# Kernel tuning notes

Measured on AMD Instinct MI355X. Metric: run time of the kernel, lower is better.

The kernel has to match this reference:

```python
import jax, jax.numpy as jnp
import numpy as np

B, S, D_MODEL, H = 2, 2048, 1024, 16
DH = D_MODEL // H  # head size = 64
NEG = -1e12


def setup_inputs() -> dict:
    key = jax.random.key(0)
    ks = jax.random.split(key, 10)
    x = jax.random.normal(ks[0], (B, S, D_MODEL), dtype=jnp.float32)
    # realistic padding mask: random valid lengths in [S//2, S]
    lengths = jax.random.randint(ks[1], (B,), S // 2, S + 1)
    mask = jnp.arange(S)[None, :] < lengths[:, None]  # [B, S] bool
    init = 0.02
    Wq = jax.random.normal(ks[2], (D_MODEL, D_MODEL), jnp.float32) * init
    Wk = jax.random.normal(ks[3], (D_MODEL, D_MODEL), jnp.float32) * init
    Wv = jax.random.normal(ks[4], (D_MODEL, D_MODEL), jnp.float32) * init
    Wr = jax.random.normal(ks[5], (D_MODEL, D_MODEL), jnp.float32) * init
    bq = jnp.zeros((D_MODEL,), jnp.float32)
    bk = jnp.zeros((D_MODEL,), jnp.float32)
    bv = jnp.zeros((D_MODEL,), jnp.float32)
    br = jnp.zeros((D_MODEL,), jnp.float32)
    return {"x": x, "mask": mask, "Wq": Wq, "bq": bq, "Wk": Wk, "bk": bk,
            "Wv": Wv, "bv": bv, "Wr": Wr, "br": br}


def reference(x, mask, Wq, bq, Wk, bk, Wv, bv, Wr, br):
    # x: [B,S,D]; mask: [B,S] bool (True = valid token)
    def heads(w, b):
        y = x @ w + b                         # [B,S,D]
        return y.reshape(B, S, H, DH).transpose(0, 2, 1, 3)  # [B,H,S,DH]

    qw, kw, vw = heads(Wq, bq), heads(Wk, bk), heads(Wv, bv)
    scores = jnp.einsum('bhqd,bhkd->bhqk', qw, kw) / jnp.sqrt(jnp.float32(DH))
    # padding mask on key axis ('-inf' fill)
    scores = jnp.where(mask[:, None, None, :], scores, NEG)
    # lm (causal, lower-triangular) additive mask
    causal = jnp.tril(jnp.ones((S, S), dtype=bool))
    scores = scores + jnp.where(causal, 0.0, NEG)[None, None]
    a = jax.nn.softmax(scores, axis=-1)
    o = jnp.einsum('bhqk,bhkd->bhqd', a, vw)          # [B,H,S,DH]
    o = o.transpose(0, 2, 1, 3).reshape(B, S, D_MODEL)  # [B,S,D]
    # second padding mask on output (value=0, sequence axis)
    o = o * mask[:, :, None].astype(o.dtype)
    # residual projection
    o = o + (x @ Wr + br)
    return o
```

## Files before the change

kernel.cpp:

```cpp
#include <hip/hip_runtime.h>
#include <hip/hip_bf16.h>

#define BQ 2
#define SEQ 2048
#define DM 1024
#define NH 16
#define DHEAD 64

typedef unsigned short u16;
typedef unsigned int u32;
typedef __attribute__((ext_vector_type(8))) short short8;
typedef __attribute__((ext_vector_type(4))) float f32x4;

__device__ __forceinline__ u16 f2b(float f) {
    unsigned u = __builtin_bit_cast(unsigned, f);
    unsigned r = u + 0x7fffu + ((u >> 16) & 1u);
    return (u16)(r >> 16);
}

__device__ __forceinline__ void gld_lds16(const void* g, void* l) {
    __builtin_amdgcn_global_load_lds(
        (const __attribute__((address_space(1))) void*)g,
        (__attribute__((address_space(3))) void*)l, 16, 0, 0);
}


__global__ __launch_bounds__(256) void cvt_x_kernel(const float* __restrict__ x,
                                                    u16* __restrict__ xb) {
    int i = blockIdx.x * 256 + threadIdx.x;
    float4 v = ((const float4*)x)[i];
    ushort4 o;
    o.x = f2b(v.x); o.y = f2b(v.y); o.z = f2b(v.z); o.w = f2b(v.w);
    ((ushort4*)xb)[i] = o;
}

__global__ __launch_bounds__(256) void pack_w4(
        const float* __restrict__ W0, const float* __restrict__ W1,
        const float* __restrict__ W2, const float* __restrict__ W3,
        u16* __restrict__ wt) {
    __shared__ u16 Ws[64][68];
    const float* W = (blockIdx.z == 0) ? W0 : (blockIdx.z == 1) ? W1
                   : (blockIdx.z == 2) ? W2 : W3;
    const int k0 = blockIdx.x * 64, d0 = blockIdx.y * 64;
    const int t = threadIdx.x;
    const int lrow = t >> 4, lcol = (t & 15) * 4;
    #pragma unroll
    for (int i = 0; i < 4; i++) {
        float4 v = *(const float4*)(W + (size_t)(k0 + lrow + i * 16) * DM + d0 + lcol);
        Ws[lrow + i * 16][lcol + 0] = f2b(v.x);
        Ws[lrow + i * 16][lcol + 1] = f2b(v.y);
        Ws[lrow + i * 16][lcol + 2] = f2b(v.z);
        Ws[lrow + i * 16][lcol + 3] = f2b(v.w);
    }
    __syncthreads();
    const int dl = t >> 2, kq = (t & 3) * 16;
    uint4 o1, o2;
    o1.x = (u32)Ws[kq + 0][dl]  | ((u32)Ws[kq + 1][dl]  << 16);
    o1.y = (u32)Ws[kq + 2][dl]  | ((u32)Ws[kq + 3][dl]  << 16);
    o1.z = (u32)Ws[kq + 4][dl]  | ((u32)Ws[kq + 5][dl]  << 16);
    o1.w = (u32)Ws[kq + 6][dl]  | ((u32)Ws[kq + 7][dl]  << 16);
    o2.x = (u32)Ws[kq + 8][dl]  | ((u32)Ws[kq + 9][dl]  << 16);
    o2.y = (u32)Ws[kq + 10][dl] | ((u32)Ws[kq + 11][dl] << 16);
    o2.z = (u32)Ws[kq + 12][dl] | ((u32)Ws[kq + 13][dl] << 16);
    o2.w = (u32)Ws[kq + 14][dl] | ((u32)Ws[kq + 15][dl] << 16);
    u16* dst = wt + (size_t)(blockIdx.z * DM + d0 + dl) * DM + k0 + kq;
    *(uint4*)(dst) = o1;
    *(uint4*)(dst + 8) = o2;
}

__global__ __launch_bounds__(256) void pack_bias_kernel(const float* __restrict__ b0,
                                                        const float* __restrict__ b1,
                                                        const float* __restrict__ b2,
                                                        const float* __restrict__ b3,
                                                        float* __restrict__ bias) {
    int i = blockIdx.x * 256 + threadIdx.x;
    const float* s = (i < 1024) ? b0 : (i < 2048) ? b1 : (i < 3072) ? b2 : b3;
    bias[i] = s[i & 1023];
}

__global__ __launch_bounds__(256) void calc_len_kernel(const int* __restrict__ mask,
                                                       int* __restrict__ lengths) {
    __shared__ int cnt[BQ];
    if (threadIdx.x < BQ) cnt[threadIdx.x] = 0;
    __syncthreads();
    for (int b = 0; b < BQ; b++) {
        int c = 0;
        for (int s = threadIdx.x; s < SEQ; s += 256)
            c += (mask[b * SEQ + s] != 0) ? 1 : 0;
        atomicAdd(&cnt[b], c);
    }
    __syncthreads();
    if (threadIdx.x < BQ) lengths[threadIdx.x] = cnt[threadIdx.x];
}


__global__ __launch_bounds__(256) void gemm_qkvr(
        const u16* __restrict__ xb, const u16* __restrict__ wt,
        const float* __restrict__ bias,
        u16* __restrict__ qbuf, u16* __restrict__ kbuf, u16* __restrict__ vbuf,
        float* __restrict__ out) {
    __shared__ __align__(16) u16 As[128 * 32];
    __shared__ __align__(16) u16 Bs[128 * 32];
    const int tid = threadIdx.x;
    const int wid = tid >> 6, lane = tid & 63;
    const int lr = lane & 15, lg = lane >> 4;
    const int bm = blockIdx.x, bn = blockIdx.y;
    const int wm = (wid >> 1) * 64, wn = (wid & 1) * 64;

    const int crow = lane >> 2, ccol = (lane & 3) * 8;
    const u16* agp0 = xb + (size_t)(bm * 128 + (wid * 2 + 0) * 16 + crow) * DM + ccol;
    const u16* agp1 = xb + (size_t)(bm * 128 + (wid * 2 + 1) * 16 + crow) * DM + ccol;
    const u16* bgp0 = wt + (size_t)(bn * 128 + (wid * 2 + 0) * 16 + crow) * DM + ccol;
    const u16* bgp1 = wt + (size_t)(bn * 128 + (wid * 2 + 1) * 16 + crow) * DM + ccol;
    u16* al0 = As + (wid * 2 + 0) * 512;
    u16* al1 = As + (wid * 2 + 1) * 512;
    u16* bl0 = Bs + (wid * 2 + 0) * 512;
    u16* bl1 = Bs + (wid * 2 + 1) * 512;

    f32x4 acc[4][4] = {};

    for (int kk = 0; kk < DM; kk += 32) {
        gld_lds16(agp0 + kk, al0);
        gld_lds16(agp1 + kk, al1);
        gld_lds16(bgp0 + kk, bl0);
        gld_lds16(bgp1 + kk, bl1);
        __syncthreads();
        short8 af[4], bfr[4];
        #pragma unroll
        for (int mt = 0; mt < 4; mt++)
            af[mt] = *(const short8*)(As + (wm + mt * 16 + lr) * 32 + lg * 8);
        #pragma unroll
        for (int nt = 0; nt < 4; nt++)
            bfr[nt] = *(const short8*)(Bs + (wn + nt * 16 + lr) * 32 + lg * 8);
        #pragma unroll
        for (int mt = 0; mt < 4; mt++)
            #pragma unroll
            for (int nt = 0; nt < 4; nt++)
                acc[mt][nt] = __builtin_amdgcn_mfma_f32_16x16x32_bf16(
                        af[mt], bfr[nt], acc[mt][nt], 0, 0, 0);
        __syncthreads();
    }

    #pragma unroll
    for (int nt = 0; nt < 4; nt++) {
        int n = bn * 128 + wn + nt * 16 + lr;
        int which = n >> 10, d = n & 1023;
        float bv_ = bias[n];
        #pragma unroll
        for (int mt = 0; mt < 4; mt++) {
            #pragma unroll
            for (int r = 0; r < 4; r++) {
                int m = bm * 128 + wm + mt * 16 + lg * 4 + r;
                float y = acc[mt][nt][r] + bv_;
                if (which == 3) {
                    out[(size_t)m * DM + d] = y;
                } else {
                    int h = d >> 6, dh = d & 63;
                    int b = m >> 11, s = m & (SEQ - 1);
                    size_t idx = ((size_t)(b * NH + h) * SEQ + s) * DHEAD + dh;
                    u16 hv = f2b(y);
                    if (which == 0) qbuf[idx] = hv;
                    else if (which == 1) kbuf[idx] = hv;
                    else vbuf[idx] = hv;
                }
            }
        }
    }
}


__global__ __launch_bounds__(128) void attn_kernel(
        const u16* __restrict__ qbuf, const u16* __restrict__ kbuf,
        const u16* __restrict__ vbuf, const int* __restrict__ lengths,
        float* __restrict__ out) {
    __shared__ __align__(16) u32 lds[2][64 * 32 + 32 * 32];

    const int wid = threadIdx.x >> 6;
    const int bh = blockIdx.x;
    const int slice = blockIdx.y;
    const int zz = blockIdx.z;
    const int qt = wid ? zz : 15 - zz;
    const int b = bh >> 4, h = bh & 15;
    const int len = lengths[b];
    const int qw = qt * 128 + slice * 32;
    if (qw >= len) return;

    u32* Vt = &lds[wid][0];
    u32* Pl = &lds[wid][2048];

    const int lane = threadIdx.x & 63;
    const int lr = lane & 15, lg = lane >> 4;
    const int swz = (lr & 7) << 2;

    const u16* qp = qbuf + (size_t)bh * SEQ * DHEAD;
    const u16* kp = kbuf + (size_t)bh * SEQ * DHEAD;
    const u16* vp = vbuf + (size_t)bh * SEQ * DHEAD;

    short8 bq[2][2];
    #pragma unroll
    for (int ntq = 0; ntq < 2; ntq++)
        #pragma unroll
        for (int ks = 0; ks < 2; ks++)
            bq[ntq][ks] = *(const short8*)(qp + (size_t)(qw + ntq * 16 + lr) * DHEAD + ks * 32 + lg * 8);

    f32x4 oacc[4][2] = {};
    float mrow[2] = {-3.0e38f, -3.0e38f};
    float lsum[2] = {0.0f, 0.0f};

    const int nkt = (qw >> 6) + 1;
    const int vk = (lane & 31) * 2;
    const int vd0 = (lane >> 5) * 8;
    const float SC = 0.125f * 1.44269504f;

    uint4 vreg[8];
    #pragma unroll
    for (int c = 0; c < 4; c++) {
        const u16* vrow = vp + (size_t)vk * DHEAD + vd0 + c * 16;
        vreg[2 * c]     = *(const uint4*)vrow;
        vreg[2 * c + 1] = *(const uint4*)(vrow + DHEAD);
    }

    for (int kt = 0; kt < nkt; kt++) {
        const int kbase = kt * 64;

        #pragma unroll
        for (int c = 0; c < 4; c++) {
            union { uint4 v; u16 sv[8]; } ua, ub;
            ua.v = vreg[2 * c]; ub.v = vreg[2 * c + 1];
            int d = vd0 + c * 16;
            #pragma unroll
            for (int j = 0; j < 8; j++) {
                u32 w = (u32)ua.sv[j] | ((u32)ub.sv[j] << 16);
                Vt[(d + j) * 32 + ((vk >> 1) ^ (j << 2))] = w;
            }
        }
        if (kt + 1 < nkt) {
            #pragma unroll
            for (int c = 0; c < 4; c++) {
                const u16* vrow = vp + (size_t)(kbase + 64 + vk) * DHEAD + vd0 + c * 16;
                vreg[2 * c]     = *(const uint4*)vrow;
                vreg[2 * c + 1] = *(const uint4*)(vrow + DHEAD);
            }
        }

        short8 ak[4][2];
        #pragma unroll
        for (int mtk = 0; mtk < 4; mtk++)
            #pragma unroll
            for (int ks = 0; ks < 2; ks++)
                ak[mtk][ks] = *(const short8*)(kp + (size_t)(kbase + mtk * 16 + lr) * DHEAD + ks * 32 + lg * 8);
        f32x4 sc[4][2] = {};
        #pragma unroll
        for (int mtk = 0; mtk < 4; mtk++)
            #pragma unroll
            for (int ks = 0; ks < 2; ks++)
                #pragma unroll
                for (int ntq = 0; ntq < 2; ntq++)
                    sc[mtk][ntq] = __builtin_amdgcn_mfma_f32_16x16x32_bf16(
                            ak[mtk][ks], bq[ntq][ks], sc[mtk][ntq], 0, 0, 0);

        const bool maskful = (kbase + 63 > qw);
        if (maskful) {
            #pragma unroll
            for (int mtk = 0; mtk < 4; mtk++) {
                int keyb = kbase + mtk * 16 + lg * 4;
                #pragma unroll
                for (int ntq = 0; ntq < 2; ntq++) {
                    int qq = qw + ntq * 16 + lr;
                    #pragma unroll
                    for (int r = 0; r < 4; r++)
                        sc[mtk][ntq][r] = (keyb + r > qq) ? -3.0e38f
                                                          : sc[mtk][ntq][r] * SC;
                }
            }
        } else {
            #pragma unroll
            for (int mtk = 0; mtk < 4; mtk++)
                #pragma unroll
                for (int ntq = 0; ntq < 2; ntq++)
                    #pragma unroll
                    for (int r = 0; r < 4; r++)
                        sc[mtk][ntq][r] *= SC;
        }

        float scl[2];
        #pragma unroll
        for (int ntq = 0; ntq < 2; ntq++) {
            float mx = sc[0][ntq][0];
            #pragma unroll
            for (int mtk = 0; mtk < 4; mtk++)
                #pragma unroll
                for (int r = 0; r < 4; r++)
                    mx = fmaxf(mx, sc[mtk][ntq][r]);
            mx = fmaxf(mx, __shfl_xor(mx, 16, 64));
            mx = fmaxf(mx, __shfl_xor(mx, 32, 64));
            float mnew = fmaxf(mrow[ntq], mx);
            float sq = exp2f(mrow[ntq] - mnew);
            mrow[ntq] = mnew;
            float ps = 0.0f;
            #pragma unroll
            for (int mtk = 0; mtk < 4; mtk++)
                #pragma unroll
                for (int r = 0; r < 4; r++) {
                    float p = exp2f(sc[mtk][ntq][r] - mnew);
                    sc[mtk][ntq][r] = p;
                    ps += p;
                }
            ps += __shfl_xor(ps, 16, 64);
            ps += __shfl_xor(ps, 32, 64);
            lsum[ntq] = lsum[ntq] * sq + ps;
            scl[ntq] = sq;
        }
        #pragma unroll
        for (int mtd = 0; mtd < 4; mtd++)
            #pragma unroll
            for (int ntq = 0; ntq < 2; ntq++)
                #pragma unroll
                for (int r = 0; r < 4; r++)
                    oacc[mtd][ntq][r] *= scl[ntq];

        #pragma unroll
        for (int ntq = 0; ntq < 2; ntq++) {
            int rowbase = (ntq * 16 + lr) * 32;
            #pragma unroll
            for (int mtk = 0; mtk < 4; mtk++)
                #pragma unroll
                for (int i = 0; i < 2; i++) {
                    u32 w = (u32)f2b(sc[mtk][ntq][2 * i])
                          | ((u32)f2b(sc[mtk][ntq][2 * i + 1]) << 16);
                    Pl[rowbase + ((mtk * 8 + lg * 2 + i) ^ swz)] = w;
                }
        }

        #pragma unroll
        for (int ks = 0; ks < 2; ks++) {
            int wv = (ks * 16 + lg * 4) ^ swz;
            short8 bp0 = *(const short8*)&Pl[(lr) * 32 + wv];
            short8 bp1 = *(const short8*)&Pl[(16 + lr) * 32 + wv];
            #pragma unroll
            for (int mtd = 0; mtd < 4; mtd++) {
                short8 av = *(const short8*)&Vt[(mtd * 16 + lr) * 32 + wv];
                oacc[mtd][0] = __builtin_amdgcn_mfma_f32_16x16x32_bf16(av, bp0, oacc[mtd][0], 0, 0, 0);
                oacc[mtd][1] = __builtin_amdgcn_mfma_f32_16x16x32_bf16(av, bp1, oacc[mtd][1], 0, 0, 0);
            }
        }
    }

    #pragma unroll
    for (int ntq = 0; ntq < 2; ntq++) {
        int q = qw + ntq * 16 + lr;
        if (q < len) {
            float inv = 1.0f / lsum[ntq];
            float* orow = out + (size_t)(b * SEQ + q) * DM + h * DHEAD;
            #pragma unroll
            for (int mtd = 0; mtd < 4; mtd++)
                #pragma unroll
                for (int r = 0; r < 4; r++)
                    orow[mtd * 16 + lg * 4 + r] += oacc[mtd][ntq][r] * inv;
        }
    }
}


extern "C" void kernel_launch(void* const* d_in, const int* in_sizes, int n_in,
                              void* d_out, int out_size, void* d_ws, size_t ws_size,
                              hipStream_t stream) {
    const float* x  = (const float*)d_in[0];
    const int*  mask = (const int*)d_in[1];
    const float* Wq = (const float*)d_in[2];
    const float* bq = (const float*)d_in[3];
    const float* Wk = (const float*)d_in[4];
    const float* bk = (const float*)d_in[5];
    const float* Wv = (const float*)d_in[6];
    const float* bv = (const float*)d_in[7];
    const float* Wr = (const float*)d_in[8];
    const float* br = (const float*)d_in[9];
    float* out = (float*)d_out;

    char* ws = (char*)d_ws;
    size_t off = 0;
    auto alloc = [&](size_t bytes) {
        size_t o = off; off = (off + bytes + 255) & ~(size_t)255; return o;
    };
    u16* xb   = (u16*)(ws + alloc((size_t)BQ * SEQ * DM * 2));
    u16* wt   = (u16*)(ws + alloc((size_t)4 * DM * DM * 2));
    float* bias = (float*)(ws + alloc(4 * DM * 4));
    u16* qbuf = (u16*)(ws + alloc((size_t)BQ * NH * SEQ * DHEAD * 2));
    u16* kbuf = (u16*)(ws + alloc((size_t)BQ * NH * SEQ * DHEAD * 2));
    u16* vbuf = (u16*)(ws + alloc((size_t)BQ * NH * SEQ * DHEAD * 2));
    int* lens = (int*)(ws + alloc(256));

    hipLaunchKernelGGL(cvt_x_kernel, dim3((BQ * SEQ * DM) / 4 / 256), dim3(256), 0, stream, x, xb);
    hipLaunchKernelGGL(pack_w4, dim3(16, 16, 4), dim3(256), 0, stream, Wq, Wk, Wv, Wr, wt);
    hipLaunchKernelGGL(pack_bias_kernel, dim3(16), dim3(256), 0, stream, bq, bk, bv, br, bias);
    hipLaunchKernelGGL(calc_len_kernel, dim3(1), dim3(256), 0, stream, mask, lens);
    hipLaunchKernelGGL(gemm_qkvr, dim3(32, 32), dim3(256), 0, stream,
                       xb, wt, bias, qbuf, kbuf, vbuf, out);
    hipLaunchKernelGGL(attn_kernel, dim3(BQ * NH, 4, 8), dim3(128), 0, stream,
                       qbuf, kbuf, vbuf, lens, out);
}
```

Before: 195.1 us.

## Split attention KV range across four waves with LDS softmax merge

Changes attention from one wave per 32-query tile (paired causal tiles per block) to four waves per 32-query tile, each processing every fourth 64-key block (split-K). The partial outputs, row maxima and row sums are merged through shared memory after a block barrier before the output is written. The grid is also remapped so consecutive block IDs spread (b,h) across XCDs. This shortens the critical path for long causal rows, at the cost of extra LDS traffic, a barrier, and idle waves on short rows.

```diff
diff --git a/kernel.cpp b/kernel.cpp
--- a/kernel.cpp
+++ b/kernel.cpp
@@ -169,28 +169,28 @@
 }
 
 
-__global__ __launch_bounds__(128) void attn_kernel(
+__global__ __launch_bounds__(256) void attn_kernel(
         const u16* __restrict__ qbuf, const u16* __restrict__ kbuf,
         const u16* __restrict__ vbuf, const int* __restrict__ lengths,
         float* __restrict__ out) {
-    __shared__ __align__(16) u32 lds[2][64 * 32 + 32 * 32];
-
-    const int wid = threadIdx.x >> 6;
-    const int bh = blockIdx.x;
-    const int slice = blockIdx.y;
-    const int zz = blockIdx.z;
-    const int qt = wid ? zz : 15 - zz;
+    __shared__ __align__(16) u32 lds[4][3072];
+    __shared__ float msh[4][32], lsh[4][32];
+
+    const int p = blockIdx.x;
+    const int xcd = p & 7, pj = p >> 3;
+    const int bh = xcd * 4 + (pj & 3);
+    const int slice = pj >> 2;
     const int b = bh >> 4, h = bh & 15;
     const int len = lengths[b];
-    const int qw = qt * 128 + slice * 32;
+    const int qw = slice * 32;
     if (qw >= len) return;
+
+    const int tid = threadIdx.x, wid = tid >> 6, lane = tid & 63;
+    const int lr = lane & 15, lg = lane >> 4;
+    const int swz = (lr & 7) << 2;
 
     u32* Vt = &lds[wid][0];
     u32* Pl = &lds[wid][2048];
-
-    const int lane = threadIdx.x & 63;
-    const int lr = lane & 15, lg = lane >> 4;
-    const int swz = (lr & 7) << 2;
 
     const u16* qp = qbuf + (size_t)bh * SEQ * DHEAD;
     const u16* kp = kbuf + (size_t)bh * SEQ * DHEAD;
@@ -207,20 +207,22 @@
     float mrow[2] = {-3.0e38f, -3.0e38f};
     float lsum[2] = {0.0f, 0.0f};
 
-    const int nkt = (qw >> 6) + 1;
+    const int last = (qw + 31) >> 6;
     const int vk = (lane & 31) * 2;
     const int vd0 = (lane >> 5) * 8;
     const float SC = 0.125f * 1.44269504f;
 
     uint4 vreg[8];
-    #pragma unroll
-    for (int c = 0; c < 4; c++) {
-        const u16* vrow = vp + (size_t)vk * DHEAD + vd0 + c * 16;
-        vreg[2 * c]     = *(const uint4*)vrow;
-        vreg[2 * c + 1] = *(const uint4*)(vrow + DHEAD);
-    }
-
-    for (int kt = 0; kt < nkt; kt++) {
+    if (wid <= last) {
+        #pragma unroll
+        for (int c = 0; c < 4; c++) {
+            const u16* vrow = vp + (size_t)(wid * 64 + vk) * DHEAD + vd0 + c * 16;
+            vreg[2 * c]     = *(const uint4*)vrow;
+            vreg[2 * c + 1] = *(const uint4*)(vrow + DHEAD);
+        }
+    }
+
+    for (int kt = wid; kt <= last; kt += 4) {
         const int kbase = kt * 64;
 
         #pragma unroll
@@ -234,10 +236,10 @@
                 Vt[(d + j) * 32 + ((vk >> 1) ^ (j << 2))] = w;
             }
         }
-        if (kt + 1 < nkt) {
+        if (kt + 4 <= last) {
             #pragma unroll
             for (int c = 0; c < 4; c++) {
-                const u16* vrow = vp + (size_t)(kbase + 64 + vk) * DHEAD + vd0 + c * 16;
+                const u16* vrow = vp + (size_t)((kt + 4) * 64 + vk) * DHEAD + vd0 + c * 16;
                 vreg[2 * c]     = *(const uint4*)vrow;
                 vreg[2 * c + 1] = *(const uint4*)(vrow + DHEAD);
             }
@@ -302,9 +304,9 @@
             for (int mtk = 0; mtk < 4; mtk++)
                 #pragma unroll
                 for (int r = 0; r < 4; r++) {
-                    float p = exp2f(sc[mtk][ntq][r] - mnew);
-                    sc[mtk][ntq][r] = p;
-                    ps += p;
+                    float pp = exp2f(sc[mtk][ntq][r] - mnew);
+                    sc[mtk][ntq][r] = pp;
+                    ps += pp;
                 }
             ps += __shfl_xor(ps, 16, 64);
             ps += __shfl_xor(ps, 32, 64);
@@ -346,17 +348,41 @@
         }
     }
 
-    #pragma unroll
-    for (int ntq = 0; ntq < 2; ntq++) {
-        int q = qw + ntq * 16 + lr;
-        if (q < len) {
-            float inv = 1.0f / lsum[ntq];
-            float* orow = out + (size_t)(b * SEQ + q) * DM + h * DHEAD;
-            #pragma unroll
-            for (int mtd = 0; mtd < 4; mtd++)
+    {
+        float* fs = (float*)&lds[wid][0];
+        #pragma unroll
+        for (int mtd = 0; mtd < 4; mtd++)
+            #pragma unroll
+            for (int ntq = 0; ntq < 2; ntq++)
                 #pragma unroll
                 for (int r = 0; r < 4; r++)
-                    orow[mtd * 16 + lg * 4 + r] += oacc[mtd][ntq][r] * inv;
+                    fs[(ntq * 16 + lr) * 64 + mtd * 16 + lg * 4 + r] = oacc[mtd][ntq][r];
+        if (lg == 0) {
+            msh[wid][lr]      = mrow[0];
+            msh[wid][16 + lr] = mrow[1];
+            lsh[wid][lr]      = lsum[0];
+            lsh[wid][16 + lr] = lsum[1];
+        }
+    }
+    __syncthreads();
+
+    {
+        const int q = tid >> 3, dblk = (tid & 7) * 8;
+        if (qw + q < len) {
+            float m0 = msh[0][q], m1 = msh[1][q], m2 = msh[2][q], m3 = msh[3][q];
+            float M = fmaxf(fmaxf(m0, m1), fmaxf(m2, m3));
+            float f0 = exp2f(m0 - M), f1 = exp2f(m1 - M);
+            float f2 = exp2f(m2 - M), f3 = exp2f(m3 - M);
+            float L = f0 * lsh[0][q] + f1 * lsh[1][q] + f2 * lsh[2][q] + f3 * lsh[3][q];
+            float inv = 1.0f / L;
+            const float* s0 = (const float*)&lds[0][0] + q * 64 + dblk;
+            float* orow = out + ((size_t)b * SEQ + qw + q) * DM + h * DHEAD + dblk;
+            #pragma unroll
+            for (int i = 0; i < 8; i++) {
+                float v = f0 * s0[i] + f1 * s0[3072 + i]
+                        + f2 * s0[6144 + i] + f3 * s0[9216 + i];
+                orow[i] += v * inv;
+            }
         }
     }
 }
@@ -396,6 +422,6 @@
     hipLaunchKernelGGL(calc_len_kernel, dim3(1), dim3(256), 0, stream, mask, lens);
     hipLaunchKernelGGL(gemm_qkvr, dim3(32, 32), dim3(256), 0, stream,
                        xb, wt, bias, qbuf, kbuf, vbuf, out);
-    hipLaunchKernelGGL(attn_kernel, dim3(BQ * NH, 4, 8), dim3(128), 0, stream,
+    hipLaunchKernelGGL(attn_kernel, dim3(BQ * NH * (SEQ / 32)), dim3(256), 0, stream,
                        qbuf, kbuf, vbuf, lens, out);
 }
```

Result: faster. 183.2 us (-6.1%).
